# Performance work log

Measured on AMD Instinct MI355X. Metric: run time of the kernel, lower is better.

## Reference

```python
import jax, jax.numpy as jnp
import numpy as np

D_MODEL = 2048
NUM_EXPERTS = 64
TOP_K = 2


def setup_inputs() -> dict:
    key = jax.random.key(0)
    kx, kw, kb = jax.random.split(key, 3)
    x = jax.random.normal(kx, (4, 4096, D_MODEL), dtype=jnp.float32)
    # nn.Linear(d_model, num_experts): weight [num_experts, d_model], bias [num_experts]
    bound = 1.0 / np.sqrt(D_MODEL)
    W = jax.random.uniform(kw, (NUM_EXPERTS, D_MODEL), minval=-bound, maxval=bound, dtype=jnp.float32)
    b = jax.random.uniform(kb, (NUM_EXPERTS,), minval=-bound, maxval=bound, dtype=jnp.float32)
    return {"x": x, "W": W, "b": b}


def reference(x, W, b):
    # Eval mode: no noise injection (self.training is False).
    logits = jnp.einsum('bsd,ed->bse', x, W) + b          # [B, S, E]
    raw_weights = jax.nn.softmax(logits, axis=-1)          # [B, S, E]
    top_k_weights, top_k_indices = jax.lax.top_k(raw_weights, TOP_K)  # [B, S, K]
    normalized = top_k_weights / jnp.sum(top_k_weights, axis=-1, keepdims=True)
    return normalized, top_k_indices
```

## Files before the change

### kernel.cpp

```cpp
#include <hip/hip_runtime.h>
#include <math.h>

#define DM 2048
#define NEXP 64
#define NTOK 16384
#define NSLICE 4
#define KSL (DM / NSLICE)
#define KC 32
#define NCH (KSL / KC)
#define MB 64
#define NBLK1 ((NTOK / MB) * NSLICE)
#define NKG (DM / KC)
#define WFRAG_BYTES (NKG * 12 * 1024)
#define PART_BYTES (NSLICE * NTOK * NEXP * 4)

typedef __attribute__((ext_vector_type(8))) short short8;
typedef __attribute__((ext_vector_type(4))) float f32x4;

__device__ __forceinline__ void async16(void* lds, const void* g) {
  __builtin_amdgcn_global_load_lds(
      (const __attribute__((address_space(1))) unsigned int*)g,
      (__attribute__((address_space(3))) unsigned int*)lds, 16, 0, 0);
}

#define PIPE_BARRIER_KEEP5() \
  asm volatile("s_waitcnt vmcnt(5)\n\ts_barrier" ::: "memory")
#define PIPE_BARRIER_DRAIN() \
  asm volatile("s_waitcnt vmcnt(0)\n\ts_barrier" ::: "memory")
#define COMPUTE_DONE_BARRIER() \
  asm volatile("s_waitcnt lgkmcnt(0)\n\ts_barrier" ::: "memory")

__device__ __forceinline__ void split3t(float f, unsigned short& h,
                                        unsigned short& m, unsigned short& l) {
  unsigned u = __float_as_uint(f);
  h = (unsigned short)(u >> 16);
  float f1 = f - __uint_as_float(u & 0xFFFF0000u);
  unsigned u1 = __float_as_uint(f1);
  m = (unsigned short)(u1 >> 16);
  float f2 = f1 - __uint_as_float(u1 & 0xFFFF0000u);
  l = (unsigned short)(__float_as_uint(f2) >> 16);
}

__device__ __forceinline__ void split8(const f32x4& a0, const f32x4& a1,
                                       short8& h, short8& m, short8& l) {
  float v[8] = {a0[0], a0[1], a0[2], a0[3], a1[0], a1[1], a1[2], a1[3]};
#pragma unroll
  for (int j = 0; j < 8; ++j) {
    unsigned short hh, mm, ll;
    split3t(v[j], hh, mm, ll);
    h[j] = (short)hh; m[j] = (short)mm; l[j] = (short)ll;
  }
}

__global__ void convw_kernel(const float* __restrict__ W,
                             unsigned short* __restrict__ wfrag) {
  const int kg = blockIdx.x;
  const int lane = threadIdx.x & 63;
  const int nt = threadIdx.x >> 6;
  const int e = nt * 16 + (lane & 15);
  const int kpos = kg * 32 + (lane >> 4) * 8;
  const f32x4* wp = (const f32x4*)(W + (size_t)e * DM + kpos);
  f32x4 w0 = wp[0], w1 = wp[1];
  short8 h, m, l;
  split8(w0, w1, h, m, l);
  size_t base = ((size_t)(kg * 12 + nt) * 64 + lane) * 8;
  *(short8*)(wfrag + base) = h;
  *(short8*)(wfrag + base + (size_t)4 * 64 * 8) = m;
  *(short8*)(wfrag + base + (size_t)8 * 64 * 8) = l;
}

__global__ __launch_bounds__(256, 4)
void router_gemm(const float* __restrict__ x,
                 const unsigned short* __restrict__ wfrag,
                 float* __restrict__ part) {
  const int lane = threadIdx.x & 63;
  const int wv = threadIdx.x >> 6;
  const int col = lane & 15;
  const int quad = lane >> 4;
  const int tg = blockIdx.x >> 2;
  const int s = blockIdx.x & 3;
  const int tok0 = tg * MB;

  __shared__ __align__(16) float xs[2][MB][KC];
  __shared__ __align__(16) unsigned short bs[2][12][64][8];

  const int xrow_in = lane >> 3;
  const int xunit = (lane & 7) ^ (xrow_in & 7);
  const float* xsrc0 =
      x + (size_t)(tok0 + wv * 16 + xrow_in) * DM + s * KSL + xunit * 4;
  const unsigned short* bsrc0 =
      wfrag + ((size_t)(s * NCH) * 12 + wv * 3) * 512 + (size_t)lane * 8;

  f32x4 acc[4];
#pragma unroll
  for (int nt = 0; nt < 4; ++nt) acc[nt] = (f32x4){0.f, 0.f, 0.f, 0.f};

  auto stage = [&](int buf, int c) {
#pragma unroll
    for (int i = 0; i < 2; ++i)
      async16(&xs[buf][wv * 16 + i * 8][0], xsrc0 + i * 8 * DM + c * KC);
#pragma unroll
    for (int q = 0; q < 3; ++q)
      async16(&bs[buf][wv * 3 + q][0][0], bsrc0 + ((size_t)c * 12 + q) * 512);
  };

  stage(0, 0);

  for (int c = 0; c < NCH; ++c) {
    const int cur = c & 1;
    if (c + 1 < NCH) {
      stage(cur ^ 1, c + 1);
      PIPE_BARRIER_KEEP5();
    } else {
      PIPE_BARRIER_DRAIN();
    }

    const int row = wv * 16 + col;
    const int u0 = (quad * 2) ^ (col & 7);
    const int u1 = (quad * 2 + 1) ^ (col & 7);
    f32x4 a0 = *(const f32x4*)&xs[cur][row][u0 * 4];
    f32x4 a1 = *(const f32x4*)&xs[cur][row][u1 * 4];
    short8 ah, am, al;
    split8(a0, a1, ah, am, al);

#pragma unroll
    for (int nt = 0; nt < 4; ++nt) {
      short8 bh = *(const short8*)&bs[cur][nt][lane][0];
      short8 bm = *(const short8*)&bs[cur][4 + nt][lane][0];
      short8 bl = *(const short8*)&bs[cur][8 + nt][lane][0];
      f32x4 cc = acc[nt];
      cc = __builtin_amdgcn_mfma_f32_16x16x32_bf16(ah, bh, cc, 0, 0, 0);
      cc = __builtin_amdgcn_mfma_f32_16x16x32_bf16(ah, bm, cc, 0, 0, 0);
      cc = __builtin_amdgcn_mfma_f32_16x16x32_bf16(am, bh, cc, 0, 0, 0);
      cc = __builtin_amdgcn_mfma_f32_16x16x32_bf16(ah, bl, cc, 0, 0, 0);
      cc = __builtin_amdgcn_mfma_f32_16x16x32_bf16(al, bh, cc, 0, 0, 0);
      cc = __builtin_amdgcn_mfma_f32_16x16x32_bf16(am, bm, cc, 0, 0, 0);
      acc[nt] = cc;
    }
    COMPUTE_DONE_BARRIER();
  }

#pragma unroll
  for (int nt = 0; nt < 4; ++nt)
#pragma unroll
    for (int r = 0; r < 4; ++r) {
      const int token = tok0 + wv * 16 + quad * 4 + r;
      part[((size_t)s * NTOK + token) * NEXP + nt * 16 + col] = acc[nt][r];
    }
}

__global__ __launch_bounds__(256, 8)
void router_reduce(const float* __restrict__ part,
                   const float* __restrict__ bias, float* __restrict__ out) {
  const int lane = threadIdx.x & 63;
  const int wv = threadIdx.x >> 6;
  const float bl = bias[lane];
  const int t0 = blockIdx.x * 8 + wv * 2;
#pragma unroll
  for (int tt = 0; tt < 2; ++tt) {
    const int t = t0 + tt;
    float v1 = bl;
#pragma unroll
    for (int sl = 0; sl < NSLICE; ++sl)
      v1 += part[((size_t)sl * NTOK + t) * NEXP + lane];
    int i1 = lane;
    float v2 = -INFINITY;
    int i2 = NEXP;
#pragma unroll
    for (int off = 32; off > 0; off >>= 1) {
      float ov1 = __shfl_xor(v1, off, 64);
      int   oi1 = __shfl_xor(i1, off, 64);
      float ov2 = __shfl_xor(v2, off, 64);
      int   oi2 = __shfl_xor(i2, off, 64);
      bool afirst = (v1 > ov1) || (v1 == ov1 && i1 < oi1);
      float w1v = afirst ? v1 : ov1;  int w1i = afirst ? i1 : oi1;
      float c1v = afirst ? v2 : ov2;  int c1i = afirst ? i2 : oi2;
      float c2v = afirst ? ov1 : v1;  int c2i = afirst ? oi1 : i1;
      bool sfirst = (c1v > c2v) || (c1v == c2v && c1i < c2i);
      v1 = w1v; i1 = w1i;
      v2 = sfirst ? c1v : c2v;
      i2 = sfirst ? c1i : c2i;
    }
    if (lane == 0) {
      const float ex = expf(v2 - v1);
      const float den = 1.f + ex;
      *(float2*)(out + 2 * t) = make_float2(1.f / den, ex / den);
      *(float2*)(out + 2 * NTOK + 2 * t) = make_float2((float)i1, (float)i2);
    }
  }
}

__global__ __launch_bounds__(512, 2)
void router_fb(const float* __restrict__ x, const float* __restrict__ W,
               const float* __restrict__ bias, float* __restrict__ out) {
  const int lane = threadIdx.x & 63;
  const int wv = threadIdx.x >> 6;
  const int col = lane & 15;
  const int quad = lane >> 4;
  const int tok0 = blockIdx.x * 32;
  const int k0 = wv * 256;

  __shared__ float part[8][32][68];

  f32x4 acc[2][4];
#pragma unroll
  for (int ms = 0; ms < 2; ++ms)
#pragma unroll
    for (int nt = 0; nt < 4; ++nt) acc[ms][nt] = (f32x4){0.f, 0.f, 0.f, 0.f};

  for (int ks = 0; ks < 8; ++ks) {
    const int k = k0 + ks * 32 + quad * 8;
    short8 ah[2], am2[2], al2[2];
#pragma unroll
    for (int ms = 0; ms < 2; ++ms) {
      const f32x4* ap = (const f32x4*)(x + (size_t)(tok0 + ms * 16 + col) * DM + k);
      f32x4 a0 = ap[0], a1 = ap[1];
      split8(a0, a1, ah[ms], am2[ms], al2[ms]);
    }
#pragma unroll
    for (int nt = 0; nt < 4; ++nt) {
      short8 bh, bm, bl;
      const f32x4* wp = (const f32x4*)(W + (size_t)(nt * 16 + col) * DM + k);
      f32x4 w0 = wp[0], w1 = wp[1];
      split8(w0, w1, bh, bm, bl);
#pragma unroll
      for (int ms = 0; ms < 2; ++ms) {
        f32x4 cc = acc[ms][nt];
        cc = __builtin_amdgcn_mfma_f32_16x16x32_bf16(ah[ms], bh, cc, 0, 0, 0);
        cc = __builtin_amdgcn_mfma_f32_16x16x32_bf16(ah[ms], bm, cc, 0, 0, 0);
        cc = __builtin_amdgcn_mfma_f32_16x16x32_bf16(am2[ms], bh, cc, 0, 0, 0);
        cc = __builtin_amdgcn_mfma_f32_16x16x32_bf16(ah[ms], bl, cc, 0, 0, 0);
        cc = __builtin_amdgcn_mfma_f32_16x16x32_bf16(al2[ms], bh, cc, 0, 0, 0);
        cc = __builtin_amdgcn_mfma_f32_16x16x32_bf16(am2[ms], bm, cc, 0, 0, 0);
        acc[ms][nt] = cc;
      }
    }
  }
#pragma unroll
  for (int ms = 0; ms < 2; ++ms)
#pragma unroll
    for (int nt = 0; nt < 4; ++nt)
#pragma unroll
      for (int r = 0; r < 4; ++r)
        part[wv][ms * 16 + quad * 4 + r][nt * 16 + col] = acc[ms][nt][r];
  __syncthreads();
  const float bl_ = bias[lane];
#pragma unroll
  for (int ti = 0; ti < 4; ++ti) {
    const int t = wv * 4 + ti;
    float v1 = bl_;
#pragma unroll
    for (int p = 0; p < 8; ++p) v1 += part[p][t][lane];
    int i1 = lane;
    float v2 = -INFINITY;
    int i2 = NEXP;
#pragma unroll
    for (int off = 32; off > 0; off >>= 1) {
      float ov1 = __shfl_xor(v1, off, 64);
      int   oi1 = __shfl_xor(i1, off, 64);
      float ov2 = __shfl_xor(v2, off, 64);
      int   oi2 = __shfl_xor(i2, off, 64);
      bool afirst = (v1 > ov1) || (v1 == ov1 && i1 < oi1);
      float w1v = afirst ? v1 : ov1;  int w1i = afirst ? i1 : oi1;
      float c1v = afirst ? v2 : ov2;  int c1i = afirst ? i2 : oi2;
      float c2v = afirst ? ov1 : v1;  int c2i = afirst ? oi1 : i1;
      bool sfirst = (c1v > c2v) || (c1v == c2v && c1i < c2i);
      v1 = w1v; i1 = w1i;
      v2 = sfirst ? c1v : c2v;
      i2 = sfirst ? c1i : c2i;
    }
    if (lane == 0) {
      const float ex = expf(v2 - v1);
      const float den = 1.f + ex;
      const int token = tok0 + t;
      *(float2*)(out + 2 * token) = make_float2(1.f / den, ex / den);
      *(float2*)(out + 2 * NTOK + 2 * token) =
          make_float2((float)i1, (float)i2);
    }
  }
}

extern "C" void kernel_launch(void* const* d_in, const int* in_sizes, int n_in,
                              void* d_out, int out_size, void* d_ws, size_t ws_size,
                              hipStream_t stream) {
  const float* x = (const float*)d_in[0];
  const float* W = (const float*)d_in[1];
  const float* b = (const float*)d_in[2];
  float* out = (float*)d_out;

  const size_t need = (size_t)WFRAG_BYTES + (size_t)PART_BYTES;
  if (ws_size >= need) {
    unsigned short* wfrag = (unsigned short*)d_ws;
    float* part = (float*)((char*)d_ws + WFRAG_BYTES);
    hipLaunchKernelGGL(convw_kernel, dim3(NKG), dim3(256), 0, stream, W, wfrag);
    hipLaunchKernelGGL(router_gemm, dim3(NBLK1), dim3(256), 0, stream,
                       x, wfrag, part);
    hipLaunchKernelGGL(router_reduce, dim3(NTOK / 8), dim3(256), 0, stream,
                       part, b, out);
  } else {
    hipLaunchKernelGGL(router_fb, dim3(NTOK / 32), dim3(512), 0, stream,
                       x, W, b, out);
  }
}
```

Before: 207.7 us.

## Give each wave private x tiles, load W fragments to registers, transpose partials

Each wave now handles 32 tokens with its own LDS double buffer for x, so block-wide barriers go away. W fragments are loaded straight from global into registers per chunk instead of being staged in LDS. Partial sums are stored expert-major so that the reduce kernel can do a per-thread sequential top-2 scan over experts with coalesced loads. The changes raise register pressure, and launch bounds drop to 2 blocks per CU. W fragments are re-read from global/L2 by every wave, and the top-2 tie-breaking order now comes from a strict greater-than scan.

```diff
diff --git a/kernel.cpp b/kernel.cpp
--- a/kernel.cpp
+++ b/kernel.cpp
@@ -8,11 +8,12 @@
 #define KSL (DM / NSLICE)
 #define KC 32
 #define NCH (KSL / KC)
-#define MB 64
-#define NBLK1 ((NTOK / MB) * NSLICE)
+#define TPW 32
+#define MBT 128
+#define NBLK1 ((NTOK / MBT) * NSLICE)
 #define NKG (DM / KC)
 #define WFRAG_BYTES (NKG * 12 * 1024)
-#define PART_BYTES (NSLICE * NTOK * NEXP * 4)
+#define PART_BYTES (NSLICE * NEXP * NTOK * 4)
 
 typedef __attribute__((ext_vector_type(8))) short short8;
 typedef __attribute__((ext_vector_type(4))) float f32x4;
@@ -22,13 +23,6 @@
       (const __attribute__((address_space(1))) unsigned int*)g,
       (__attribute__((address_space(3))) unsigned int*)lds, 16, 0, 0);
 }
-
-#define PIPE_BARRIER_KEEP5() \
-  asm volatile("s_waitcnt vmcnt(5)\n\ts_barrier" ::: "memory")
-#define PIPE_BARRIER_DRAIN() \
-  asm volatile("s_waitcnt vmcnt(0)\n\ts_barrier" ::: "memory")
-#define COMPUTE_DONE_BARRIER() \
-  asm volatile("s_waitcnt lgkmcnt(0)\n\ts_barrier" ::: "memory")
 
 __device__ __forceinline__ void split3t(float f, unsigned short& h,
                                         unsigned short& m, unsigned short& l) {
@@ -69,7 +63,7 @@
   *(short8*)(wfrag + base + (size_t)8 * 64 * 8) = l;
 }
 
-__global__ __launch_bounds__(256, 4)
+__global__ __launch_bounds__(256, 2)
 void router_gemm(const float* __restrict__ x,
                  const unsigned short* __restrict__ wfrag,
                  float* __restrict__ part) {
@@ -79,90 +73,176 @@
   const int quad = lane >> 4;
   const int tg = blockIdx.x >> 2;
   const int s = blockIdx.x & 3;
-  const int tok0 = tg * MB;
-
-  __shared__ __align__(16) float xs[2][MB][KC];
-  __shared__ __align__(16) unsigned short bs[2][12][64][8];
-
-  const int xrow_in = lane >> 3;
-  const int xunit = (lane & 7) ^ (xrow_in & 7);
-  const float* xsrc0 =
-      x + (size_t)(tok0 + wv * 16 + xrow_in) * DM + s * KSL + xunit * 4;
-  const unsigned short* bsrc0 =
-      wfrag + ((size_t)(s * NCH) * 12 + wv * 3) * 512 + (size_t)lane * 8;
-
-  f32x4 acc[4];
-#pragma unroll
-  for (int nt = 0; nt < 4; ++nt) acc[nt] = (f32x4){0.f, 0.f, 0.f, 0.f};
+  const int tok0 = tg * MBT + wv * TPW;
+
+  __shared__ __align__(16) float xs[4][2][TPW][KC];
+
+  const int rowoff = lane >> 3;
+  const int unit = (lane & 7) ^ (rowoff & 7);
+  const float* xsrc = x + (size_t)(tok0 + rowoff) * DM + s * KSL + unit * 4;
 
   auto stage = [&](int buf, int c) {
 #pragma unroll
-    for (int i = 0; i < 2; ++i)
-      async16(&xs[buf][wv * 16 + i * 8][0], xsrc0 + i * 8 * DM + c * KC);
-#pragma unroll
-    for (int q = 0; q < 3; ++q)
-      async16(&bs[buf][wv * 3 + q][0][0], bsrc0 + ((size_t)c * 12 + q) * 512);
+    for (int i = 0; i < 4; ++i)
+      async16(&xs[wv][buf][i * 8][0], xsrc + (size_t)(i * 8) * DM + c * KC);
   };
+
+  f32x4 acc[2][4];
+#pragma unroll
+  for (int mt = 0; mt < 2; ++mt)
+#pragma unroll
+    for (int nt = 0; nt < 4; ++nt) acc[mt][nt] = (f32x4){0.f, 0.f, 0.f, 0.f};
+
+  const unsigned short* bbase = wfrag + (size_t)(s * NCH) * 12 * 512 +
+                                (size_t)lane * 8;
 
   stage(0, 0);
 
   for (int c = 0; c < NCH; ++c) {
     const int cur = c & 1;
+
+    short8 B[3][4];
+#pragma unroll
+    for (int limb = 0; limb < 3; ++limb)
+#pragma unroll
+      for (int nt = 0; nt < 4; ++nt)
+        B[limb][nt] = *(const short8*)(bbase +
+            ((size_t)c * 12 + limb * 4 + nt) * 512);
+
+    asm volatile("" ::: "memory");
+
     if (c + 1 < NCH) {
       stage(cur ^ 1, c + 1);
-      PIPE_BARRIER_KEEP5();
+      asm volatile("s_waitcnt vmcnt(16)" ::: "memory");
     } else {
-      PIPE_BARRIER_DRAIN();
-    }
-
-    const int row = wv * 16 + col;
-    const int u0 = (quad * 2) ^ (col & 7);
-    const int u1 = (quad * 2 + 1) ^ (col & 7);
-    f32x4 a0 = *(const f32x4*)&xs[cur][row][u0 * 4];
-    f32x4 a1 = *(const f32x4*)&xs[cur][row][u1 * 4];
-    short8 ah, am, al;
-    split8(a0, a1, ah, am, al);
-
+      asm volatile("s_waitcnt vmcnt(12)" ::: "memory");
+    }
+
+#pragma unroll
+    for (int mt = 0; mt < 2; ++mt) {
+      const int row = mt * 16 + col;
+      const int u0 = (quad * 2) ^ (col & 7);
+      const int u1 = (quad * 2 + 1) ^ (col & 7);
+      f32x4 a0 = *(const f32x4*)&xs[wv][cur][row][u0 * 4];
+      f32x4 a1 = *(const f32x4*)&xs[wv][cur][row][u1 * 4];
+      short8 ah, am, al;
+      split8(a0, a1, ah, am, al);
+#pragma unroll
+      for (int nt = 0; nt < 4; ++nt) {
+        f32x4 cc = acc[mt][nt];
+        cc = __builtin_amdgcn_mfma_f32_16x16x32_bf16(ah, B[0][nt], cc, 0, 0, 0);
+        cc = __builtin_amdgcn_mfma_f32_16x16x32_bf16(ah, B[1][nt], cc, 0, 0, 0);
+        cc = __builtin_amdgcn_mfma_f32_16x16x32_bf16(am, B[0][nt], cc, 0, 0, 0);
+        cc = __builtin_amdgcn_mfma_f32_16x16x32_bf16(ah, B[2][nt], cc, 0, 0, 0);
+        cc = __builtin_amdgcn_mfma_f32_16x16x32_bf16(al, B[0][nt], cc, 0, 0, 0);
+        cc = __builtin_amdgcn_mfma_f32_16x16x32_bf16(am, B[1][nt], cc, 0, 0, 0);
+        acc[mt][nt] = cc;
+      }
+    }
+  }
+
+#pragma unroll
+  for (int mt = 0; mt < 2; ++mt)
 #pragma unroll
     for (int nt = 0; nt < 4; ++nt) {
-      short8 bh = *(const short8*)&bs[cur][nt][lane][0];
-      short8 bm = *(const short8*)&bs[cur][4 + nt][lane][0];
-      short8 bl = *(const short8*)&bs[cur][8 + nt][lane][0];
-      f32x4 cc = acc[nt];
-      cc = __builtin_amdgcn_mfma_f32_16x16x32_bf16(ah, bh, cc, 0, 0, 0);
-      cc = __builtin_amdgcn_mfma_f32_16x16x32_bf16(ah, bm, cc, 0, 0, 0);
-      cc = __builtin_amdgcn_mfma_f32_16x16x32_bf16(am, bh, cc, 0, 0, 0);
-      cc = __builtin_amdgcn_mfma_f32_16x16x32_bf16(ah, bl, cc, 0, 0, 0);
-      cc = __builtin_amdgcn_mfma_f32_16x16x32_bf16(al, bh, cc, 0, 0, 0);
-      cc = __builtin_amdgcn_mfma_f32_16x16x32_bf16(am, bm, cc, 0, 0, 0);
-      acc[nt] = cc;
-    }
-    COMPUTE_DONE_BARRIER();
-  }
-
-#pragma unroll
-  for (int nt = 0; nt < 4; ++nt)
-#pragma unroll
-    for (int r = 0; r < 4; ++r) {
-      const int token = tok0 + wv * 16 + quad * 4 + r;
-      part[((size_t)s * NTOK + token) * NEXP + nt * 16 + col] = acc[nt][r];
-    }
-}
-
-__global__ __launch_bounds__(256, 8)
+      const size_t e = (size_t)(s * NEXP + nt * 16 + col);
+      *(f32x4*)(part + e * NTOK + tok0 + mt * 16 + quad * 4) = acc[mt][nt];
+    }
+}
+
+__global__ __launch_bounds__(256, 4)
 void router_reduce(const float* __restrict__ part,
                    const float* __restrict__ bias, float* __restrict__ out) {
   const int lane = threadIdx.x & 63;
   const int wv = threadIdx.x >> 6;
-  const float bl = bias[lane];
-  const int t0 = blockIdx.x * 8 + wv * 2;
-#pragma unroll
-  for (int tt = 0; tt < 2; ++tt) {
-    const int t = t0 + tt;
-    float v1 = bl;
-#pragma unroll
-    for (int sl = 0; sl < NSLICE; ++sl)
-      v1 += part[((size_t)sl * NTOK + t) * NEXP + lane];
+  const int q = lane >> 4;
+  const int t = blockIdx.x * 64 + wv * 16 + (lane & 15);
+
+  float v1 = -INFINITY, v2 = -INFINITY;
+  int i1 = 0, i2 = 0;
+#pragma unroll
+  for (int e = 0; e < NEXP; ++e) {
+    float p = part[(size_t)(q * NEXP + e) * NTOK + t];
+    p += __shfl_xor(p, 16, 64);
+    p += __shfl_xor(p, 32, 64);
+    const float v = p + bias[e];
+    const bool a = v > v1;
+    const bool b = v > v2;
+    const float nv2 = a ? v1 : (b ? v : v2);
+    const int ni2 = a ? i1 : (b ? e : i2);
+    v2 = nv2; i2 = ni2;
+    i1 = a ? e : i1;
+    v1 = a ? v : v1;
+  }
+  if (q == 0) {
+    const float ex = expf(v2 - v1);
+    const float den = 1.f + ex;
+    *(float2*)(out + 2 * t) = make_float2(1.f / den, ex / den);
+    *(float2*)(out + 2 * NTOK + 2 * t) = make_float2((float)i1, (float)i2);
+  }
+}
+
+__global__ __launch_bounds__(512, 2)
+void router_fb(const float* __restrict__ x, const float* __restrict__ W,
+               const float* __restrict__ bias, float* __restrict__ out) {
+  const int lane = threadIdx.x & 63;
+  const int wv = threadIdx.x >> 6;
+  const int col = lane & 15;
+  const int quad = lane >> 4;
+  const int tok0 = blockIdx.x * 32;
+  const int k0 = wv * 256;
+
+  __shared__ float part[8][32][68];
+
+  f32x4 acc[2][4];
+#pragma unroll
+  for (int ms = 0; ms < 2; ++ms)
+#pragma unroll
+    for (int nt = 0; nt < 4; ++nt) acc[ms][nt] = (f32x4){0.f, 0.f, 0.f, 0.f};
+
+  for (int ks = 0; ks < 8; ++ks) {
+    const int k = k0 + ks * 32 + quad * 8;
+    short8 ah[2], am2[2], al2[2];
+#pragma unroll
+    for (int ms = 0; ms < 2; ++ms) {
+      const f32x4* ap = (const f32x4*)(x + (size_t)(tok0 + ms * 16 + col) * DM + k);
+      f32x4 a0 = ap[0], a1 = ap[1];
+      split8(a0, a1, ah[ms], am2[ms], al2[ms]);
+    }
+#pragma unroll
+    for (int nt = 0; nt < 4; ++nt) {
+      short8 bh, bm, bl;
+      const f32x4* wp = (const f32x4*)(W + (size_t)(nt * 16 + col) * DM + k);
+      f32x4 w0 = wp[0], w1 = wp[1];
+      split8(w0, w1, bh, bm, bl);
+#pragma unroll
+      for (int ms = 0; ms < 2; ++ms) {
+        f32x4 cc = acc[ms][nt];
+        cc = __builtin_amdgcn_mfma_f32_16x16x32_bf16(ah[ms], bh, cc, 0, 0, 0);
+        cc = __builtin_amdgcn_mfma_f32_16x16x32_bf16(ah[ms], bm, cc, 0, 0, 0);
+        cc = __builtin_amdgcn_mfma_f32_16x16x32_bf16(am2[ms], bh, cc, 0, 0, 0);
+        cc = __builtin_amdgcn_mfma_f32_16x16x32_bf16(ah[ms], bl, cc, 0, 0, 0);
+        cc = __builtin_amdgcn_mfma_f32_16x16x32_bf16(al2[ms], bh, cc, 0, 0, 0);
+        cc = __builtin_amdgcn_mfma_f32_16x16x32_bf16(am2[ms], bm, cc, 0, 0, 0);
+        acc[ms][nt] = cc;
+      }
+    }
+  }
+#pragma unroll
+  for (int ms = 0; ms < 2; ++ms)
+#pragma unroll
+    for (int nt = 0; nt < 4; ++nt)
+#pragma unroll
+      for (int r = 0; r < 4; ++r)
+        part[wv][ms * 16 + quad * 4 + r][nt * 16 + col] = acc[ms][nt][r];
+  __syncthreads();
+  const float bl_ = bias[lane];
+#pragma unroll
+  for (int ti = 0; ti < 4; ++ti) {
+    const int t = wv * 4 + ti;
+    float v1 = bl_;
+#pragma unroll
+    for (int p = 0; p < 8; ++p) v1 += part[p][t][lane];
     int i1 = lane;
     float v2 = -INFINITY;
     int i2 = NEXP;
@@ -184,94 +264,6 @@
     if (lane == 0) {
       const float ex = expf(v2 - v1);
       const float den = 1.f + ex;
-      *(float2*)(out + 2 * t) = make_float2(1.f / den, ex / den);
-      *(float2*)(out + 2 * NTOK + 2 * t) = make_float2((float)i1, (float)i2);
-    }
-  }
-}
-
-__global__ __launch_bounds__(512, 2)
-void router_fb(const float* __restrict__ x, const float* __restrict__ W,
-               const float* __restrict__ bias, float* __restrict__ out) {
-  const int lane = threadIdx.x & 63;
-  const int wv = threadIdx.x >> 6;
-  const int col = lane & 15;
-  const int quad = lane >> 4;
-  const int tok0 = blockIdx.x * 32;
-  const int k0 = wv * 256;
-
-  __shared__ float part[8][32][68];
-
-  f32x4 acc[2][4];
-#pragma unroll
-  for (int ms = 0; ms < 2; ++ms)
-#pragma unroll
-    for (int nt = 0; nt < 4; ++nt) acc[ms][nt] = (f32x4){0.f, 0.f, 0.f, 0.f};
-
-  for (int ks = 0; ks < 8; ++ks) {
-    const int k = k0 + ks * 32 + quad * 8;
-    short8 ah[2], am2[2], al2[2];
-#pragma unroll
-    for (int ms = 0; ms < 2; ++ms) {
-      const f32x4* ap = (const f32x4*)(x + (size_t)(tok0 + ms * 16 + col) * DM + k);
-      f32x4 a0 = ap[0], a1 = ap[1];
-      split8(a0, a1, ah[ms], am2[ms], al2[ms]);
-    }
-#pragma unroll
-    for (int nt = 0; nt < 4; ++nt) {
-      short8 bh, bm, bl;
-      const f32x4* wp = (const f32x4*)(W + (size_t)(nt * 16 + col) * DM + k);
-      f32x4 w0 = wp[0], w1 = wp[1];
-      split8(w0, w1, bh, bm, bl);
-#pragma unroll
-      for (int ms = 0; ms < 2; ++ms) {
-        f32x4 cc = acc[ms][nt];
-        cc = __builtin_amdgcn_mfma_f32_16x16x32_bf16(ah[ms], bh, cc, 0, 0, 0);
-        cc = __builtin_amdgcn_mfma_f32_16x16x32_bf16(ah[ms], bm, cc, 0, 0, 0);
-        cc = __builtin_amdgcn_mfma_f32_16x16x32_bf16(am2[ms], bh, cc, 0, 0, 0);
-        cc = __builtin_amdgcn_mfma_f32_16x16x32_bf16(ah[ms], bl, cc, 0, 0, 0);
-        cc = __builtin_amdgcn_mfma_f32_16x16x32_bf16(al2[ms], bh, cc, 0, 0, 0);
-        cc = __builtin_amdgcn_mfma_f32_16x16x32_bf16(am2[ms], bm, cc, 0, 0, 0);
-        acc[ms][nt] = cc;
-      }
-    }
-  }
-#pragma unroll
-  for (int ms = 0; ms < 2; ++ms)
-#pragma unroll
-    for (int nt = 0; nt < 4; ++nt)
-#pragma unroll
-      for (int r = 0; r < 4; ++r)
-        part[wv][ms * 16 + quad * 4 + r][nt * 16 + col] = acc[ms][nt][r];
-  __syncthreads();
-  const float bl_ = bias[lane];
-#pragma unroll
-  for (int ti = 0; ti < 4; ++ti) {
-    const int t = wv * 4 + ti;
-    float v1 = bl_;
-#pragma unroll
-    for (int p = 0; p < 8; ++p) v1 += part[p][t][lane];
-    int i1 = lane;
-    float v2 = -INFINITY;
-    int i2 = NEXP;
-#pragma unroll
-    for (int off = 32; off > 0; off >>= 1) {
-      float ov1 = __shfl_xor(v1, off, 64);
-      int   oi1 = __shfl_xor(i1, off, 64);
-      float ov2 = __shfl_xor(v2, off, 64);
-      int   oi2 = __shfl_xor(i2, off, 64);
-      bool afirst = (v1 > ov1) || (v1 == ov1 && i1 < oi1);
-      float w1v = afirst ? v1 : ov1;  int w1i = afirst ? i1 : oi1;
-      float c1v = afirst ? v2 : ov2;  int c1i = afirst ? i2 : oi2;
-      float c2v = afirst ? ov1 : v1;  int c2i = afirst ? oi1 : i1;
-      bool sfirst = (c1v > c2v) || (c1v == c2v && c1i < c2i);
-      v1 = w1v; i1 = w1i;
-      v2 = sfirst ? c1v : c2v;
-      i2 = sfirst ? c1i : c2i;
-    }
-    if (lane == 0) {
-      const float ex = expf(v2 - v1);
-      const float den = 1.f + ex;
       const int token = tok0 + t;
       *(float2*)(out + 2 * token) = make_float2(1.f / den, ex / den);
       *(float2*)(out + 2 * NTOK + 2 * token) =
@@ -295,7 +287,7 @@
     hipLaunchKernelGGL(convw_kernel, dim3(NKG), dim3(256), 0, stream, W, wfrag);
     hipLaunchKernelGGL(router_gemm, dim3(NBLK1), dim3(256), 0, stream,
                        x, wfrag, part);
-    hipLaunchKernelGGL(router_reduce, dim3(NTOK / 8), dim3(256), 0, stream,
+    hipLaunchKernelGGL(router_reduce, dim3(NTOK / 64), dim3(256), 0, stream,
                        part, b, out);
   } else {
     hipLaunchKernelGGL(router_fb, dim3(NTOK / 32), dim3(512), 0, stream,
```

After: 210.1 us. Within noise of the previous version (+1.1%).
